# Performance work log

Hardware: AMD Instinct MI355X
Metric: run time of the kernel (lower is better)

Reference implementation:

```python
import jax, jax.numpy as jnp
import numpy as np

B, T, C, H = 2, 2048, 1024, 16
D = C // H  # head dim = 64


def setup_inputs() -> dict:
    key = jax.random.key(0)
    ks = jax.random.split(key, 9)
    s = 1.0 / np.sqrt(C)
    x = jax.random.normal(ks[0], (B, T, C), dtype=jnp.float32)
    # causal lower-triangular mask, broadcast over heads: [B, 1, T, T]
    attn_mask = jnp.broadcast_to(jnp.tril(jnp.ones((T, T), dtype=jnp.int32)), (B, 1, T, T))
    Wq = jax.random.normal(ks[1], (C, C), dtype=jnp.float32) * s
    Wk = jax.random.normal(ks[2], (C, C), dtype=jnp.float32) * s
    Wv = jax.random.normal(ks[3], (C, C), dtype=jnp.float32) * s
    Wo = jax.random.normal(ks[4], (C, C), dtype=jnp.float32) * s
    bq = jax.random.normal(ks[5], (C,), dtype=jnp.float32) * s
    bk = jax.random.normal(ks[6], (C,), dtype=jnp.float32) * s
    bv = jax.random.normal(ks[7], (C,), dtype=jnp.float32) * s
    bo = jax.random.normal(ks[8], (C,), dtype=jnp.float32) * s
    return {"x": x, "attn_mask": attn_mask, "Wq": Wq, "bq": bq, "Wk": Wk, "bk": bk,
            "Wv": Wv, "bv": bv, "Wo": Wo, "bo": bo}


def reference(x, attn_mask, Wq, bq, Wk, bk, Wv, bv, Wo, bo):
    # Q/K/V projections: nn.Linear applies x @ W^T + b
    def split_heads(t):  # [B,T,C] -> [B,H,T,D]
        return t.reshape(B, T, H, D).transpose(0, 2, 1, 3)

    q = split_heads(x @ Wq.T + bq)
    k = split_heads(x @ Wk.T + bk)
    v = split_heads(x @ Wv.T + bv)

    scale = 1.0 / np.sqrt(D)
    att = jnp.einsum('bhqd,bhkd->bhqk', q, k) * scale  # [B,H,T,T]
    att = jnp.where(attn_mask[:, :, :T, :T] == 0, -jnp.inf, att)
    att = jax.nn.softmax(att, axis=-1)
    # dropout p=0.0 -> identity
    y = jnp.einsum('bhqk,bhkd->bhqd', att, v)  # [B,H,T,D]
    y = y.transpose(0, 2, 1, 3).reshape(B, T, C)
    return y @ Wo.T + bo
```

## Files before the change

kernel.cpp:

```cpp
#include <hip/hip_runtime.h>
#include <hip/hip_bf16.h>

#define B_ 2
#define T_ 2048
#define C_ 1024
#define H_ 16
#define D_ 64
#define BT_ (B_ * T_)
#define S3_ 3072

typedef __bf16 bf16x8 __attribute__((ext_vector_type(8)));
typedef short short8 __attribute__((ext_vector_type(8)));
typedef float f32x4 __attribute__((ext_vector_type(4)));

__device__ inline bf16x8 ld_frag_bf(const short* p) {
    short8 s = *(const short8*)p;
    return __builtin_bit_cast(bf16x8, s);
}
__device__ inline bf16x8 ld_frag_f32(const float* p) {
    f32x4 a = *(const f32x4*)p;
    f32x4 b = *(const f32x4*)(p + 4);
    bf16x8 r;
#pragma unroll
    for (int i = 0; i < 4; ++i) { r[i] = (__bf16)a[i]; r[i + 4] = (__bf16)b[i]; }
    return r;
}
__device__ inline short f2bf(float f) {
    union { float f; unsigned u; } x;
    x.f = f;
    unsigned r = x.u + 0x7fff + ((x.u >> 16) & 1);
    return (short)(r >> 16);
}
__device__ inline void st_out(short* p, float v) { *p = f2bf(v); }
__device__ inline void st_out(float* p, float v) { *p = v; }

__device__ inline void async16(const void* g, void* l) {
    __builtin_amdgcn_global_load_lds(
        (const __attribute__((address_space(1))) unsigned*)g,
        (__attribute__((address_space(3))) unsigned*)l, 16, 0, 0);
}

__global__ __launch_bounds__(256) void conv_weights(
    const float* __restrict__ Wq, const float* __restrict__ Wk,
    const float* __restrict__ Wv, const float* __restrict__ Wo,
    short* __restrict__ Wqkvb, short* __restrict__ Wob)
{
    size_t e = ((size_t)blockIdx.x * 256 + threadIdx.x) * 8;
    int r = (int)(e >> 20);
    size_t off = e & ((1u << 20) - 1);
    const float* src = (r == 0) ? Wq : (r == 1) ? Wk : (r == 2) ? Wv : Wo;
    short* dst = (r < 3) ? (Wqkvb + ((size_t)r << 20) + off) : (Wob + off);
    f32x4 a = *(const f32x4*)(src + off);
    f32x4 b = *(const f32x4*)(src + off + 4);
    short8 s;
#pragma unroll
    for (int i = 0; i < 4; ++i) { s[i] = f2bf(a[i]); s[i + 4] = f2bf(b[i]); }
    *(short8*)dst = s;
}

template <typename AT, typename OT>
__global__ __launch_bounds__(256) void gemm_m97(
    const AT* __restrict__ A, int lda,
    const short* __restrict__ Wb,
    const float* __restrict__ b0, const float* __restrict__ b1,
    const float* __restrict__ b2,
    OT* __restrict__ Out, int ldo)
{
    constexpr int K = 1024;
    __shared__ __align__(16) short Bs[128 * 32];
    __shared__ __align__(16) AT As[128 * 32];

    const int tid = threadIdx.x;
    const int w = tid >> 6, l = tid & 63;
    const int c = l & 15, qd = l >> 4;
    const int m0 = blockIdx.y * 128, n0 = blockIdx.x * 128;
    const int wm = w >> 1, wn = w & 1;

    const float* bias = (n0 < 1024) ? b0 : (n0 < 2048 ? b1 : b2);

    f32x4 acc[4][4] = {};

    for (int k0 = 0; k0 < K; k0 += 32) {
#pragma unroll
        for (int p = 0; p < 2; ++p) {
            int row = p * 64 + w * 16 + (l >> 2);
            const short* g = Wb + (size_t)(n0 + row) * K + k0 + (l & 3) * 8;
            short* lp = Bs + p * 2048 + w * 512 + l * 8;
            async16(g, lp);
        }
        if constexpr (sizeof(AT) == 2) {
#pragma unroll
            for (int p = 0; p < 2; ++p) {
                int row = p * 64 + w * 16 + (l >> 2);
                const AT* g = A + (size_t)(m0 + row) * lda + k0 + (l & 3) * 8;
                AT* lp = As + p * 2048 + w * 512 + l * 8;
                async16(g, lp);
            }
        } else {
#pragma unroll
            for (int p = 0; p < 4; ++p) {
                int row = p * 32 + w * 8 + (l >> 3);
                const AT* g = A + (size_t)(m0 + row) * lda + k0 + (l & 7) * 4;
                AT* lp = As + p * 1024 + w * 256 + l * 4;
                async16(g, lp);
            }
        }
        __syncthreads();

        bf16x8 af[4], bfr[4];
#pragma unroll
        for (int i = 0; i < 4; ++i) {
            int rowa = wm * 64 + i * 16 + c;
            if constexpr (sizeof(AT) == 2)
                af[i] = ld_frag_bf((const short*)As + rowa * 32 + qd * 8);
            else
                af[i] = ld_frag_f32((const float*)As + rowa * 32 + qd * 8);
            int rowb = wn * 64 + i * 16 + c;
            bfr[i] = ld_frag_bf(Bs + rowb * 32 + qd * 8);
        }
#pragma unroll
        for (int i = 0; i < 4; ++i)
#pragma unroll
            for (int j = 0; j < 4; ++j)
                acc[i][j] = __builtin_amdgcn_mfma_f32_16x16x32_bf16(af[i], bfr[j], acc[i][j], 0, 0, 0);
        __syncthreads();
    }

#pragma unroll
    for (int i = 0; i < 4; ++i)
#pragma unroll
        for (int j = 0; j < 4; ++j) {
            int n = n0 + wn * 64 + j * 16 + c;
            float bv = bias[n & 1023];
#pragma unroll
            for (int r = 0; r < 4; ++r) {
                int m = m0 + wm * 64 + i * 16 + qd * 4 + r;
                st_out(Out + (size_t)m * ldo + n, acc[i][j][r] + bv);
            }
        }
}

__global__ __launch_bounds__(256) void attn_flash3(short* __restrict__ QKV)
{
    __shared__ __align__(16) short Ksm[2][64 * 64];
    __shared__ __align__(16) short Vsm[2][64 * 72];
    __shared__ __align__(16) short Psm[4][16 * 72];

    const int tid = threadIdx.x;
    const int w = tid >> 6, l = tid & 63;
    const int c = l & 15, qd = l >> 4;
    const int pair = blockIdx.x;
    const int bh = blockIdx.y;
    const int b = bh >> 4, h = bh & 15;

    short* Qbase = QKV + (size_t)b * T_ * S3_ + h * 64;
    const short* Kbase = Qbase + 1024;
    const short* Vbase = Qbase + 2048;

#pragma unroll 1
    for (int seg = 0; seg < 2; ++seg) {
        const int qt = (seg == 0) ? pair : 31 - pair;
        const int q0 = qt * 64, wq0 = q0 + w * 16;

        bf16x8 aq0 = ld_frag_bf(Qbase + (size_t)(wq0 + c) * S3_ + qd * 8);
        bf16x8 aq1 = ld_frag_bf(Qbase + (size_t)(wq0 + c) * S3_ + 32 + qd * 8);

        f32x4 o[4] = {};
        float lrow[4] = {0.f, 0.f, 0.f, 0.f};

        {
#pragma unroll
            for (int p = 0; p < 2; ++p) {
                int row = p * 32 + w * 8 + (l >> 3);
                async16(Kbase + (size_t)row * S3_ + (l & 7) * 8,
                        &Ksm[0][row * 64 + (l & 7) * 8]);
            }
            const short* g = Vbase + (size_t)l * S3_ + w * 16;
            short8 v0 = *(const short8*)g;
            short8 v1 = *(const short8*)(g + 8);
#pragma unroll
            for (int e = 0; e < 8; ++e) {
                Vsm[0][(w * 16 + e) * 72 + l]     = v0[e];
                Vsm[0][(w * 16 + 8 + e) * 72 + l] = v1[e];
            }
        }
        __syncthreads();

#pragma unroll 1
        for (int kt = 0; kt <= qt; ++kt) {
            const int cur = kt & 1;
            const int k0 = kt * 64;

            short8 nv0, nv1;
            if (kt < qt) {
#pragma unroll
                for (int p = 0; p < 2; ++p) {
                    int row = p * 32 + w * 8 + (l >> 3);
                    async16(Kbase + (size_t)(k0 + 64 + row) * S3_ + (l & 7) * 8,
                            &Ksm[1 - cur][row * 64 + (l & 7) * 8]);
                }
                const short* g = Vbase + (size_t)(k0 + 64 + l) * S3_ + w * 16;
                nv0 = *(const short8*)g;
                nv1 = *(const short8*)(g + 8);
            }

            f32x4 s[4];
#pragma unroll
            for (int j = 0; j < 4; ++j) {
                s[j] = (f32x4){0.f, 0.f, 0.f, 0.f};
                bf16x8 kb0 = ld_frag_bf(&Ksm[cur][(j * 16 + c) * 64 + qd * 8]);
                bf16x8 kb1 = ld_frag_bf(&Ksm[cur][(j * 16 + c) * 64 + 32 + qd * 8]);
                s[j] = __builtin_amdgcn_mfma_f32_16x16x32_bf16(aq0, kb0, s[j], 0, 0, 0);
                s[j] = __builtin_amdgcn_mfma_f32_16x16x32_bf16(aq1, kb1, s[j], 0, 0, 0);
            }

            const bool diag = (kt == qt);
            float p_[4][4];
#pragma unroll
            for (int r = 0; r < 4; ++r) {
                const int qrow = wq0 + qd * 4 + r;
                float acc = 0.f;
#pragma unroll
                for (int j = 0; j < 4; ++j) {
                    float p = __expf(fmaf(s[j][r], 0.125f, -8.0f));
                    if (diag && (k0 + j * 16 + c > qrow)) p = 0.f;
                    p_[r][j] = p;
                    acc += p;
                }
                lrow[r] += acc;
            }

            short* P = Psm[w];
#pragma unroll
            for (int r = 0; r < 4; ++r)
#pragma unroll
                for (int j = 0; j < 4; ++j)
                    P[(qd * 4 + r) * 72 + j * 16 + c] = f2bf(p_[r][j]);

            if (kt < qt) {
#pragma unroll
                for (int e = 0; e < 8; ++e) {
                    Vsm[1 - cur][(w * 16 + e) * 72 + l]     = nv0[e];
                    Vsm[1 - cur][(w * 16 + 8 + e) * 72 + l] = nv1[e];
                }
            }

            bf16x8 pa0 = ld_frag_bf(P + c * 72 + qd * 8);
            bf16x8 pa1 = ld_frag_bf(P + c * 72 + 32 + qd * 8);
#pragma unroll
            for (int j = 0; j < 4; ++j) {
                bf16x8 vb0 = ld_frag_bf(&Vsm[cur][(j * 16 + c) * 72 + qd * 8]);
                bf16x8 vb1 = ld_frag_bf(&Vsm[cur][(j * 16 + c) * 72 + 32 + qd * 8]);
                o[j] = __builtin_amdgcn_mfma_f32_16x16x32_bf16(pa0, vb0, o[j], 0, 0, 0);
                o[j] = __builtin_amdgcn_mfma_f32_16x16x32_bf16(pa1, vb1, o[j], 0, 0, 0);
            }
            __syncthreads();
        }

        float inv[4];
#pragma unroll
        for (int r = 0; r < 4; ++r) {
            float s = lrow[r];
            s += __shfl_xor(s, 1);
            s += __shfl_xor(s, 2);
            s += __shfl_xor(s, 4);
            s += __shfl_xor(s, 8);
            inv[r] = 1.0f / s;
        }

#pragma unroll
        for (int j = 0; j < 4; ++j)
#pragma unroll
            for (int r = 0; r < 4; ++r) {
                int qrow = wq0 + qd * 4 + r;
                Qbase[(size_t)qrow * S3_ + j * 16 + c] = f2bf(o[j][r] * inv[r]);
            }
    }
}

extern "C" void kernel_launch(void* const* d_in, const int* in_sizes, int n_in,
                              void* d_out, int out_size, void* d_ws, size_t ws_size,
                              hipStream_t stream)
{
    const float* x  = (const float*)d_in[0];
    const float* Wq = (const float*)d_in[2];
    const float* bq = (const float*)d_in[3];
    const float* Wk = (const float*)d_in[4];
    const float* bk = (const float*)d_in[5];
    const float* Wv = (const float*)d_in[6];
    const float* bv = (const float*)d_in[7];
    const float* Wo = (const float*)d_in[8];
    const float* bo = (const float*)d_in[9];
    float* out = (float*)d_out;

    short* QKVs  = (short*)d_ws;
    short* Wqkvb = QKVs + (size_t)BT_ * S3_;
    short* Wob   = Wqkvb + (size_t)S3_ * C_;

    conv_weights<<<2048, 256, 0, stream>>>(Wq, Wk, Wv, Wo, Wqkvb, Wob);
    gemm_m97<float, short><<<dim3(S3_ / 128, BT_ / 128), 256, 0, stream>>>(
        x, C_, Wqkvb, bq, bk, bv, QKVs, S3_);
    attn_flash3<<<dim3(16, B_ * H_), 256, 0, stream>>>(QKVs);
    gemm_m97<short, float><<<dim3(C_ / 128, BT_ / 128), 256, 0, stream>>>(
        QKVs, S3_, Wob, bo, bo, bo, out, C_);
}
```

Before: 243.5 us.

## Pre-convert x to bf16 and XOR-swizzle K tiles in attention shared memory

The conversion kernel now also turns the activation x into bf16, storing it temporarily in the output buffer. The QKV GEMM then loads A as bf16 through the same async path as the weights, which halves A traffic and drops the per-fragment float-to-bf16 conversion. In the attention kernel, K tiles are written into shared memory with an XOR swizzle on 16-byte chunks and read back with the matching swizzle, to avoid LDS bank conflicts. The cost is an extra pass over x and a workspace reuse of the output buffer.

```diff
diff --git a/kernel.cpp b/kernel.cpp
--- a/kernel.cpp
+++ b/kernel.cpp
@@ -17,14 +17,6 @@
     short8 s = *(const short8*)p;
     return __builtin_bit_cast(bf16x8, s);
 }
-__device__ inline bf16x8 ld_frag_f32(const float* p) {
-    f32x4 a = *(const f32x4*)p;
-    f32x4 b = *(const f32x4*)(p + 4);
-    bf16x8 r;
-#pragma unroll
-    for (int i = 0; i < 4; ++i) { r[i] = (__bf16)a[i]; r[i + 4] = (__bf16)b[i]; }
-    return r;
-}
 __device__ inline short f2bf(float f) {
     union { float f; unsigned u; } x;
     x.f = f;
@@ -40,27 +32,31 @@
         (__attribute__((address_space(3))) unsigned*)l, 16, 0, 0);
 }
 
-__global__ __launch_bounds__(256) void conv_weights(
+__global__ __launch_bounds__(256) void conv_inputs(
+    const float* __restrict__ x,
     const float* __restrict__ Wq, const float* __restrict__ Wk,
     const float* __restrict__ Wv, const float* __restrict__ Wo,
-    short* __restrict__ Wqkvb, short* __restrict__ Wob)
+    short* __restrict__ xb, short* __restrict__ Wqkvb, short* __restrict__ Wob)
 {
     size_t e = ((size_t)blockIdx.x * 256 + threadIdx.x) * 8;
     int r = (int)(e >> 20);
     size_t off = e & ((1u << 20) - 1);
-    const float* src = (r == 0) ? Wq : (r == 1) ? Wk : (r == 2) ? Wv : Wo;
-    short* dst = (r < 3) ? (Wqkvb + ((size_t)r << 20) + off) : (Wob + off);
-    f32x4 a = *(const f32x4*)(src + off);
-    f32x4 b = *(const f32x4*)(src + off + 4);
+    const float* src; short* dst;
+    if (r < 4)      { src = x + e;  dst = xb + e; }
+    else if (r < 7) { src = (r == 4 ? Wq : r == 5 ? Wk : Wv) + off;
+                      dst = Wqkvb + ((size_t)(r - 4) << 20) + off; }
+    else            { src = Wo + off; dst = Wob + off; }
+    f32x4 a = *(const f32x4*)src;
+    f32x4 b = *(const f32x4*)(src + 4);
     short8 s;
 #pragma unroll
     for (int i = 0; i < 4; ++i) { s[i] = f2bf(a[i]); s[i + 4] = f2bf(b[i]); }
     *(short8*)dst = s;
 }
 
-template <typename AT, typename OT>
+template <typename OT>
 __global__ __launch_bounds__(256) void gemm_m97(
-    const AT* __restrict__ A, int lda,
+    const short* __restrict__ A, int lda,
     const short* __restrict__ Wb,
     const float* __restrict__ b0, const float* __restrict__ b1,
     const float* __restrict__ b2,
@@ -68,7 +64,7 @@
 {
     constexpr int K = 1024;
     __shared__ __align__(16) short Bs[128 * 32];
-    __shared__ __align__(16) AT As[128 * 32];
+    __shared__ __align__(16) short As[128 * 32];
 
     const int tid = threadIdx.x;
     const int w = tid >> 6, l = tid & 63;
@@ -84,39 +80,18 @@
 #pragma unroll
         for (int p = 0; p < 2; ++p) {
             int row = p * 64 + w * 16 + (l >> 2);
-            const short* g = Wb + (size_t)(n0 + row) * K + k0 + (l & 3) * 8;
-            short* lp = Bs + p * 2048 + w * 512 + l * 8;
-            async16(g, lp);
-        }
-        if constexpr (sizeof(AT) == 2) {
-#pragma unroll
-            for (int p = 0; p < 2; ++p) {
-                int row = p * 64 + w * 16 + (l >> 2);
-                const AT* g = A + (size_t)(m0 + row) * lda + k0 + (l & 3) * 8;
-                AT* lp = As + p * 2048 + w * 512 + l * 8;
-                async16(g, lp);
-            }
-        } else {
-#pragma unroll
-            for (int p = 0; p < 4; ++p) {
-                int row = p * 32 + w * 8 + (l >> 3);
-                const AT* g = A + (size_t)(m0 + row) * lda + k0 + (l & 7) * 4;
-                AT* lp = As + p * 1024 + w * 256 + l * 4;
-                async16(g, lp);
-            }
+            async16(Wb + (size_t)(n0 + row) * K + k0 + (l & 3) * 8,
+                    Bs + p * 2048 + w * 512 + l * 8);
+            async16(A + (size_t)(m0 + row) * lda + k0 + (l & 3) * 8,
+                    As + p * 2048 + w * 512 + l * 8);
         }
         __syncthreads();
 
         bf16x8 af[4], bfr[4];
 #pragma unroll
         for (int i = 0; i < 4; ++i) {
-            int rowa = wm * 64 + i * 16 + c;
-            if constexpr (sizeof(AT) == 2)
-                af[i] = ld_frag_bf((const short*)As + rowa * 32 + qd * 8);
-            else
-                af[i] = ld_frag_f32((const float*)As + rowa * 32 + qd * 8);
-            int rowb = wn * 64 + i * 16 + c;
-            bfr[i] = ld_frag_bf(Bs + rowb * 32 + qd * 8);
+            af[i]  = ld_frag_bf(As + (wm * 64 + i * 16 + c) * 32 + qd * 8);
+            bfr[i] = ld_frag_bf(Bs + (wn * 64 + i * 16 + c) * 32 + qd * 8);
         }
 #pragma unroll
         for (int i = 0; i < 4; ++i)
@@ -140,7 +115,7 @@
         }
 }
 
-__global__ __launch_bounds__(256) void attn_flash3(short* __restrict__ QKV)
+__global__ __launch_bounds__(256) void attn_flash4(short* __restrict__ QKV)
 {
     __shared__ __align__(16) short Ksm[2][64 * 64];
     __shared__ __align__(16) short Vsm[2][64 * 72];
@@ -152,6 +127,7 @@
     const int pair = blockIdx.x;
     const int bh = blockIdx.y;
     const int b = bh >> 4, h = bh & 15;
+    const int sw = c & 7;
 
     short* Qbase = QKV + (size_t)b * T_ * S3_ + h * 64;
     const short* Kbase = Qbase + 1024;
@@ -172,7 +148,8 @@
 #pragma unroll
             for (int p = 0; p < 2; ++p) {
                 int row = p * 32 + w * 8 + (l >> 3);
-                async16(Kbase + (size_t)row * S3_ + (l & 7) * 8,
+                int srcC = (l & 7) ^ (row & 7);
+                async16(Kbase + (size_t)row * S3_ + srcC * 8,
                         &Ksm[0][row * 64 + (l & 7) * 8]);
             }
             const short* g = Vbase + (size_t)l * S3_ + w * 16;
@@ -196,7 +173,8 @@
 #pragma unroll
                 for (int p = 0; p < 2; ++p) {
                     int row = p * 32 + w * 8 + (l >> 3);
-                    async16(Kbase + (size_t)(k0 + 64 + row) * S3_ + (l & 7) * 8,
+                    int srcC = (l & 7) ^ (row & 7);
+                    async16(Kbase + (size_t)(k0 + 64 + row) * S3_ + srcC * 8,
                             &Ksm[1 - cur][row * 64 + (l & 7) * 8]);
                 }
                 const short* g = Vbase + (size_t)(k0 + 64 + l) * S3_ + w * 16;
@@ -208,8 +186,9 @@
 #pragma unroll
             for (int j = 0; j < 4; ++j) {
                 s[j] = (f32x4){0.f, 0.f, 0.f, 0.f};
-                bf16x8 kb0 = ld_frag_bf(&Ksm[cur][(j * 16 + c) * 64 + qd * 8]);
-                bf16x8 kb1 = ld_frag_bf(&Ksm[cur][(j * 16 + c) * 64 + 32 + qd * 8]);
+                const short* kr = &Ksm[cur][(j * 16 + c) * 64];
+                bf16x8 kb0 = ld_frag_bf(kr + (qd ^ sw) * 8);
+                bf16x8 kb1 = ld_frag_bf(kr + (qd ^ 4 ^ sw) * 8);
                 s[j] = __builtin_amdgcn_mfma_f32_16x16x32_bf16(aq0, kb0, s[j], 0, 0, 0);
                 s[j] = __builtin_amdgcn_mfma_f32_16x16x32_bf16(aq1, kb1, s[j], 0, 0, 0);
             }
@@ -296,11 +275,12 @@
     short* QKVs  = (short*)d_ws;
     short* Wqkvb = QKVs + (size_t)BT_ * S3_;
     short* Wob   = Wqkvb + (size_t)S3_ * C_;
-
-    conv_weights<<<2048, 256, 0, stream>>>(Wq, Wk, Wv, Wo, Wqkvb, Wob);
-    gemm_m97<float, short><<<dim3(S3_ / 128, BT_ / 128), 256, 0, stream>>>(
-        x, C_, Wqkvb, bq, bk, bv, QKVs, S3_);
-    attn_flash3<<<dim3(16, B_ * H_), 256, 0, stream>>>(QKVs);
-    gemm_m97<short, float><<<dim3(C_ / 128, BT_ / 128), 256, 0, stream>>>(
+    short* xb    = (short*)d_out;
+
+    conv_inputs<<<4096, 256, 0, stream>>>(x, Wq, Wk, Wv, Wo, xb, Wqkvb, Wob);
+    gemm_m97<short><<<dim3(S3_ / 128, BT_ / 128), 256, 0, stream>>>(
+        xb, C_, Wqkvb, bq, bk, bv, QKVs, S3_);
+    attn_flash4<<<dim3(16, B_ * H_), 256, 0, stream>>>(QKVs);
+    gemm_m97<float><<<dim3(C_ / 128, BT_ / 128), 256, 0, stream>>>(
         QKVs, S3_, Wob, bo, bo, bo, out, C_);
 }
```

After: 227.6 us. 6.5% less time.
